# Optimization experiments

Hardware: AMD Instinct MI355X
Metric: run time of the kernel (lower is better)

## Reference

```python
import math
import jax, jax.numpy as jnp
import numpy as np

D_MODEL = 2048
NUM_EXPERTS = 64
Z_LOSS_COEF = 1e-3
AUX_LOSS_COEF = 1e-2
CAPACITY_FACTOR = 1.0
MIN_CAPACITY = 4


def setup_inputs() -> dict:
    key = jax.random.key(0)
    kx, kw = jax.random.split(key)
    x = jax.random.normal(kx, (4, 4096, D_MODEL), dtype=jnp.float32)
    W = 0.02 * jax.random.normal(kw, (NUM_EXPERTS, D_MODEL), dtype=jnp.float32)  # gate weight [E, D]
    return {"x": x, "W": W}


def reference(x, W):
    B, T, D = x.shape
    N = B * T                      # num_tokens
    E = W.shape[0]
    x_flat = x.reshape(N, D)

    logits = jnp.einsum("nd,ed->ne", x_flat, W)          # gate GEMM [N, E]
    probs = jax.nn.softmax(logits, axis=-1)

    # z-loss: mean(logsumexp(logits)^2)
    z_loss = jnp.mean(jnp.square(jax.nn.logsumexp(logits, axis=-1)))

    expert_index = jnp.argmax(logits, axis=-1)            # [N] int
    expert_prob = jnp.take_along_axis(probs, expert_index[:, None], axis=-1)[:, 0]  # [N]

    counts = jnp.bincount(expert_index, length=E)         # [E] int
    f_i = counts.astype(probs.dtype) / N                  # fraction routed per expert
    p_i = jnp.mean(probs, axis=0)                         # mean router prob per expert
    aux_loss = AUX_LOSS_COEF * E * jnp.sum(f_i * p_i) + Z_LOSS_COEF * z_loss

    capacity = max(MIN_CAPACITY, math.ceil(CAPACITY_FACTOR * N / E))  # static int
    return expert_index, expert_prob, counts, capacity, aux_loss
```

## Files before the change

### kernel.cpp

```cpp
#include <hip/hip_runtime.h>
#include <math.h>

#define D_MODEL 2048
#define NE      64
#define TB      64
#define KSEG    1024
#define KC      64
#define NCH     (KSEG / KC)
#define FB_KC   32
#define FB_NCH  (D_MODEL / FB_KC)

typedef _Float16 half8 __attribute__((ext_vector_type(8)));
typedef float    f32x4 __attribute__((ext_vector_type(4)));

#define CVT1(F, HV, LV, J) do {                                               \
    float _f = (F);                                                           \
    _Float16 _h = (_Float16)_f;                                               \
    HV[J] = _h;                                                               \
    LV[J] = (_Float16)(_f - (float)_h);                                       \
} while (0)

__global__ __launch_bounds__(256) void wcvt_kernel(
    const float* __restrict__ W, short* __restrict__ Wh, short* __restrict__ Wl)
{
    const int e = blockIdx.x, t = threadIdx.x, c = t * 8;
    const float* src = W + (size_t)e * D_MODEL + c;
    float4 v0 = *(const float4*)src;
    float4 v1 = *(const float4*)(src + 4);
    half8 hv, lv;
    CVT1(v0.x * 64.0f, hv, lv, 0); CVT1(v0.y * 64.0f, hv, lv, 1);
    CVT1(v0.z * 64.0f, hv, lv, 2); CVT1(v0.w * 64.0f, hv, lv, 3);
    CVT1(v1.x * 64.0f, hv, lv, 4); CVT1(v1.y * 64.0f, hv, lv, 5);
    CVT1(v1.z * 64.0f, hv, lv, 6); CVT1(v1.w * 64.0f, hv, lv, 7);
    *(half8*)(Wh + (size_t)e * D_MODEL + c) = hv;
    *(half8*)(Wl + (size_t)e * D_MODEL + c) = lv;
}

__global__ __launch_bounds__(512) void router_fused_db(
    const float* __restrict__ x, const short* __restrict__ Whg,
    const short* __restrict__ Wlg, float* __restrict__ out,
    float* __restrict__ ws_prob, float* __restrict__ ws_z,
    int* __restrict__ ws_cnt, int Ntok)
{
    __shared__ __align__(16) char smem[131072];

    const int t  = threadIdx.x;
    const int b  = blockIdx.x;
    const int m0 = b * TB;
    const int g  = t >> 8;
    const int tg = t & 255;
    const int l  = tg & 63;
    const int wv = tg >> 6;
    const int k0 = g * KSEG;

    char* gbase = smem + g * 65536;

    float (*sL)[NE + 1] = (float (*)[NE + 1])smem;
    float (*red8)[8]    = (float (*)[8])(smem + 16640);
    int   (*arg8)[8]    = (int (*)[8])(smem + 18688);
    float* smax         = (float*)(smem + 20736);
    float* sinv         = (float*)(smem + 20992);
    float (*spart)[NE]  = (float (*)[NE])(smem + 21248);
    int*   hist         = (int*)(smem + 23296);

    const int srow = tg >> 2;
    const int sc   = tg & 3;
    const int ssw  = srow & 7;
    const int sof0 = (srow << 6) + (((sc * 2 + 0) ^ ssw) << 3);
    const int sof1 = (srow << 6) + (((sc * 2 + 1) ^ ssw) << 3);

    float4 aA0, aA1, aA2, aA3;
    float4 aB0, aB1, aB2, aB3;
    uint4  whA0, whA1, wlA0, wlA1;
    uint4  whB0, whB1, wlB0, wlB1;

#define PRE_SET(A0, A1, A2, A3, WH0, WH1, WL0, WL1, KB) do {                  \
    const float* _ap = x + (size_t)(m0 + srow) * D_MODEL + (KB) + sc * 16;    \
    A0 = *(const float4*)_ap;       A1 = *(const float4*)(_ap + 4);           \
    A2 = *(const float4*)(_ap + 8); A3 = *(const float4*)(_ap + 12);          \
    const size_t _wr = (size_t)srow * D_MODEL + (KB) + sc * 16;               \
    WH0 = *(const uint4*)&Whg[_wr]; WH1 = *(const uint4*)&Whg[_wr + 8];       \
    WL0 = *(const uint4*)&Wlg[_wr]; WL1 = *(const uint4*)&Wlg[_wr + 8];       \
} while (0)

#define STORE_SET(A0, A1, A2, A3, WH0, WH1, WL0, WL1, BB) do {                \
    _Float16* _Ah = (_Float16*)(gbase + (BB) * 32768);                        \
    _Float16* _Al = (_Float16*)(gbase + (BB) * 32768 + 8192);                 \
    _Float16* _Wh = (_Float16*)(gbase + (BB) * 32768 + 16384);                \
    _Float16* _Wl = (_Float16*)(gbase + (BB) * 32768 + 24576);                \
    half8 _h0, _l0, _h1, _l1;                                                 \
    CVT1((A0).x * 8.0f, _h0, _l0, 0); CVT1((A0).y * 8.0f, _h0, _l0, 1);       \
    CVT1((A0).z * 8.0f, _h0, _l0, 2); CVT1((A0).w * 8.0f, _h0, _l0, 3);       \
    CVT1((A1).x * 8.0f, _h0, _l0, 4); CVT1((A1).y * 8.0f, _h0, _l0, 5);       \
    CVT1((A1).z * 8.0f, _h0, _l0, 6); CVT1((A1).w * 8.0f, _h0, _l0, 7);       \
    CVT1((A2).x * 8.0f, _h1, _l1, 0); CVT1((A2).y * 8.0f, _h1, _l1, 1);       \
    CVT1((A2).z * 8.0f, _h1, _l1, 2); CVT1((A2).w * 8.0f, _h1, _l1, 3);       \
    CVT1((A3).x * 8.0f, _h1, _l1, 4); CVT1((A3).y * 8.0f, _h1, _l1, 5);       \
    CVT1((A3).z * 8.0f, _h1, _l1, 6); CVT1((A3).w * 8.0f, _h1, _l1, 7);       \
    *(half8*)&_Ah[sof0] = _h0;  *(half8*)&_Ah[sof1] = _h1;                    \
    *(half8*)&_Al[sof0] = _l0;  *(half8*)&_Al[sof1] = _l1;                    \
    *(uint4*)&_Wh[sof0] = WH0;  *(uint4*)&_Wh[sof1] = WH1;                    \
    *(uint4*)&_Wl[sof0] = WL0;  *(uint4*)&_Wl[sof1] = WL1;                    \
} while (0)

#define MFMA_PHASE(BB) do {                                                   \
    const _Float16* _Ah = (const _Float16*)(gbase + (BB) * 32768);            \
    const _Float16* _Al = (const _Float16*)(gbase + (BB) * 32768 + 8192);     \
    const _Float16* _Wh = (const _Float16*)(gbase + (BB) * 32768 + 16384);    \
    const _Float16* _Wl = (const _Float16*)(gbase + (BB) * 32768 + 24576);    \
    const int arow = wv * 16 + (l & 15);                                      \
    const int rsw  = l & 7;                                                   \
    _Pragma("unroll")                                                         \
    for (int kq = 0; kq < 2; ++kq) {                                          \
        const int s    = kq * 4 + (l >> 4);                                   \
        const int aoff = arow * 64 + ((s ^ rsw) << 3);                        \
        half8 ah = *(const half8*)&_Ah[aoff];                                 \
        half8 al = *(const half8*)&_Al[aoff];                                 \
        _Pragma("unroll")                                                     \
        for (int n = 0; n < 4; ++n) {                                         \
            const int woff = (n * 16 + (l & 15)) * 64 + ((s ^ rsw) << 3);     \
            half8 wh = *(const half8*)&_Wh[woff];                             \
            half8 wl = *(const half8*)&_Wl[woff];                             \
            f32x4 a = (n == 0) ? acc0 : (n == 1) ? acc1 : (n == 2) ? acc2 : acc3; \
            a = __builtin_amdgcn_mfma_f32_16x16x32_f16(al, wl, a, 0, 0, 0);   \
            a = __builtin_amdgcn_mfma_f32_16x16x32_f16(al, wh, a, 0, 0, 0);   \
            a = __builtin_amdgcn_mfma_f32_16x16x32_f16(ah, wl, a, 0, 0, 0);   \
            a = __builtin_amdgcn_mfma_f32_16x16x32_f16(ah, wh, a, 0, 0, 0);   \
            if (n == 0) acc0 = a; else if (n == 1) acc1 = a;                  \
            else if (n == 2) acc2 = a; else acc3 = a;                         \
        }                                                                     \
    }                                                                         \
} while (0)

    f32x4 acc0 = {0.f,0.f,0.f,0.f}, acc1 = {0.f,0.f,0.f,0.f};
    f32x4 acc2 = {0.f,0.f,0.f,0.f}, acc3 = {0.f,0.f,0.f,0.f};

    PRE_SET(aA0, aA1, aA2, aA3, whA0, whA1, wlA0, wlA1, k0);
    PRE_SET(aB0, aB1, aB2, aB3, whB0, whB1, wlB0, wlB1, k0 + KC);
    STORE_SET(aA0, aA1, aA2, aA3, whA0, whA1, wlA0, wlA1, 0);
    asm volatile("s_waitcnt lgkmcnt(0)" ::: "memory");
    __builtin_amdgcn_s_barrier();

    for (int ch = 0; ch < NCH; ch += 2) {
        if (ch + 2 < NCH)
            PRE_SET(aA0, aA1, aA2, aA3, whA0, whA1, wlA0, wlA1, k0 + (ch + 2) * KC);
        if (ch + 1 < NCH)
            STORE_SET(aB0, aB1, aB2, aB3, whB0, whB1, wlB0, wlB1, 1);
        MFMA_PHASE(0);
        asm volatile("s_waitcnt lgkmcnt(0)" ::: "memory");
        __builtin_amdgcn_s_barrier();
        if (ch + 3 < NCH)
            PRE_SET(aB0, aB1, aB2, aB3, whB0, whB1, wlB0, wlB1, k0 + (ch + 3) * KC);
        if (ch + 2 < NCH)
            STORE_SET(aA0, aA1, aA2, aA3, whA0, whA1, wlA0, wlA1, 0);
        MFMA_PHASE(1);
        asm volatile("s_waitcnt lgkmcnt(0)" ::: "memory");
        __builtin_amdgcn_s_barrier();
    }

    __syncthreads();
    const int rbase = wv * 16 + (l >> 4) * 4;
    const int col0  = l & 15;
    if (g == 1) {
        #pragma unroll
        for (int q = 0; q < 4; ++q) {
            sL[rbase + q][ 0 + col0] = acc0[q];
            sL[rbase + q][16 + col0] = acc1[q];
            sL[rbase + q][32 + col0] = acc2[q];
            sL[rbase + q][48 + col0] = acc3[q];
        }
    }
    __syncthreads();
    if (g == 0) {
        #pragma unroll
        for (int q = 0; q < 4; ++q) {
            sL[rbase + q][ 0 + col0] = (acc0[q] + sL[rbase + q][ 0 + col0]) * (1.0f / 512.0f);
            sL[rbase + q][16 + col0] = (acc1[q] + sL[rbase + q][16 + col0]) * (1.0f / 512.0f);
            sL[rbase + q][32 + col0] = (acc2[q] + sL[rbase + q][32 + col0]) * (1.0f / 512.0f);
            sL[rbase + q][48 + col0] = (acc3[q] + sL[rbase + q][48 + col0]) * (1.0f / 512.0f);
        }
    }
    if (t < NE) hist[t] = 0;
    __syncthreads();

    {
        const int m = t >> 3, qr = t & 7;
        float mx = -3.4e38f; int ag = qr * 8;
        #pragma unroll
        for (int k = 0; k < 8; ++k) {
            const int e = qr * 8 + k;
            float v = sL[m][e];
            if (v > mx) { mx = v; ag = e; }
        }
        red8[m][qr] = mx; arg8[m][qr] = ag;
    }
    __syncthreads();
    if (t < 64) {
        const int m = t;
        float mx = red8[m][0]; int ag = arg8[m][0];
        #pragma unroll
        for (int qr = 1; qr < 8; ++qr)
            if (red8[m][qr] > mx) { mx = red8[m][qr]; ag = arg8[m][qr]; }
        smax[m] = mx;
        out[m0 + m] = (float)ag;
        atomicAdd(&hist[ag], 1);
    }
    __syncthreads();
    {
        const int m = t >> 3, qr = t & 7;
        const float mx = smax[m];
        float s = 0.f;
        #pragma unroll
        for (int k = 0; k < 8; ++k) s += expf(sL[m][qr * 8 + k] - mx);
        red8[m][qr] = s;
    }
    __syncthreads();
    if (t < 64) {
        const int m = t;
        float s = 0.f;
        #pragma unroll
        for (int qr = 0; qr < 8; ++qr) s += red8[m][qr];
        float inv = 1.f / s;
        sinv[m] = inv;
        out[Ntok + m0 + m] = inv;
        float lse = smax[m] + logf(s);
        float z = lse * lse;
        #pragma unroll
        for (int off = 32; off > 0; off >>= 1) z += __shfl_down(z, off, 64);
        if (t == 0) ws_z[b] = z;
    }
    __syncthreads();
    {
        const int e = t & 63, gw = t >> 6;
        float pa = 0.f;
        #pragma unroll
        for (int k = 0; k < 8; ++k) {
            const int m = gw * 8 + k;
            pa += expf(sL[m][e] - smax[m]) * sinv[m];
        }
        spart[gw][e] = pa;
    }
    __syncthreads();
    if (t < NE) {
        float ps = 0.f;
        #pragma unroll
        for (int gw = 0; gw < 8; ++gw) ps += spart[gw][t];
        ws_prob[b * NE + t] = ps;
        ws_cnt[b * NE + t]  = hist[t];
    }
}

__global__ __launch_bounds__(256) void router_final2(
    const float* __restrict__ ws_prob, const float* __restrict__ ws_z,
    const int* __restrict__ ws_cnt, float* __restrict__ out,
    int Ntok, int nblocks)
{
    __shared__ float sp[4][NE];
    __shared__ int   sc[4][NE];
    __shared__ float sz[4];

    const int e = threadIdx.x & 63, g = threadIdx.x >> 6;
    const int per = nblocks / 4;
    const int hi  = (g == 3) ? nblocks : (g + 1) * per;

    float ps = 0.f; int c = 0;
    for (int blk = g * per; blk < hi; ++blk) {
        ps += ws_prob[blk * NE + e];
        c  += ws_cnt[blk * NE + e];
    }
    sp[g][e] = ps; sc[g][e] = c;

    float z = 0.f;
    for (int blk = (int)threadIdx.x; blk < nblocks; blk += 256) z += ws_z[blk];
    #pragma unroll
    for (int off = 32; off > 0; off >>= 1) z += __shfl_down(z, off, 64);
    if (e == 0) sz[g] = z;
    __syncthreads();

    if (threadIdx.x < 64) {
        const int ee = threadIdx.x;
        float pst = ((sp[0][ee] + sp[1][ee]) + sp[2][ee]) + sp[3][ee];
        int   ct  = ((sc[0][ee] + sc[1][ee]) + sc[2][ee]) + sc[3][ee];
        out[2 * Ntok + ee] = (float)ct;

        float fN = (float)Ntok;
        float fp = ((float)ct / fN) * (pst / fN);
        #pragma unroll
        for (int off = 32; off > 0; off >>= 1) fp += __shfl_down(fp, off, 64);
        if (ee == 0) {
            float zt = ((sz[0] + sz[1]) + sz[2]) + sz[3];
            int cap = (Ntok + NE - 1) / NE;
            if (cap < 4) cap = 4;
            float aux = 0.01f * (float)NE * fp + 1e-3f * (zt / fN);
            out[2 * Ntok + NE]     = (float)cap;
            out[2 * Ntok + NE + 1] = aux;
        }
    }
}

__global__ __launch_bounds__(256) void router_main_fb(
    const float* __restrict__ x, const float* __restrict__ W,
    float* __restrict__ out, float* __restrict__ ws_prob,
    float* __restrict__ ws_z, int* __restrict__ ws_cnt, int Ntok)
{
    __shared__ __align__(16) float sX[FB_KC][68];
    __shared__ __align__(16) float sW[FB_KC][68];
    __shared__ float sL[64][65];
    __shared__ float smax[64], sinv[64];
    __shared__ float spart[4][NE];
    __shared__ int   hist[NE];

    const int t = threadIdx.x, b = blockIdx.x, m0 = b * 64;
    const int mq = t & 15, nq = t >> 4;
    const int r1 = t >> 3, r2 = r1 + 32, c1 = (t & 7) << 2;
    const float* xp1 = x + (size_t)(m0 + r1) * D_MODEL + c1;
    const float* xp2 = x + (size_t)(m0 + r2) * D_MODEL + c1;
    const float* wp1 = W + (size_t)r1 * D_MODEL + c1;
    const float* wp2 = W + (size_t)r2 * D_MODEL + c1;
    float4 ax1 = *(const float4*)xp1, ax2 = *(const float4*)xp2;
    float4 aw1 = *(const float4*)wp1, aw2 = *(const float4*)wp2;
    float a1[4][4] = {}, a2[4][4] = {};
    for (int ch = 0; ch < FB_NCH; ++ch) {
        __syncthreads();
        sX[c1+0][r1] = ax1.x; sX[c1+1][r1] = ax1.y; sX[c1+2][r1] = ax1.z; sX[c1+3][r1] = ax1.w;
        sX[c1+0][r2] = ax2.x; sX[c1+1][r2] = ax2.y; sX[c1+2][r2] = ax2.z; sX[c1+3][r2] = ax2.w;
        sW[c1+0][r1] = aw1.x; sW[c1+1][r1] = aw1.y; sW[c1+2][r1] = aw1.z; sW[c1+3][r1] = aw1.w;
        sW[c1+0][r2] = aw2.x; sW[c1+1][r2] = aw2.y; sW[c1+2][r2] = aw2.z; sW[c1+3][r2] = aw2.w;
        __syncthreads();
        if (ch + 1 < FB_NCH) {
            xp1 += FB_KC; xp2 += FB_KC; wp1 += FB_KC; wp2 += FB_KC;
            ax1 = *(const float4*)xp1; ax2 = *(const float4*)xp2;
            aw1 = *(const float4*)wp1; aw2 = *(const float4*)wp2;
        }
        #pragma unroll
        for (int k = 0; k < FB_KC; ++k) {
            float4 xa = *(const float4*)&sX[k][mq << 2];
            float4 wb = *(const float4*)&sW[k][nq << 2];
            float (*A)[4] = (k < FB_KC / 2) ? a1 : a2;
            A[0][0] = fmaf(xa.x, wb.x, A[0][0]); A[0][1] = fmaf(xa.x, wb.y, A[0][1]);
            A[0][2] = fmaf(xa.x, wb.z, A[0][2]); A[0][3] = fmaf(xa.x, wb.w, A[0][3]);
            A[1][0] = fmaf(xa.y, wb.x, A[1][0]); A[1][1] = fmaf(xa.y, wb.y, A[1][1]);
            A[1][2] = fmaf(xa.y, wb.z, A[1][2]); A[1][3] = fmaf(xa.y, wb.w, A[1][3]);
            A[2][0] = fmaf(xa.z, wb.x, A[2][0]); A[2][1] = fmaf(xa.z, wb.y, A[2][1]);
            A[2][2] = fmaf(xa.z, wb.z, A[2][2]); A[2][3] = fmaf(xa.z, wb.w, A[2][3]);
            A[3][0] = fmaf(xa.w, wb.x, A[3][0]); A[3][1] = fmaf(xa.w, wb.y, A[3][1]);
            A[3][2] = fmaf(xa.w, wb.z, A[3][2]); A[3][3] = fmaf(xa.w, wb.w, A[3][3]);
        }
    }
    #pragma unroll
    for (int i = 0; i < 4; ++i)
        #pragma unroll
        for (int j = 0; j < 4; ++j)
            sL[(mq << 2) + i][(nq << 2) + j] = a1[i][j] + a2[i][j];
    if (t < NE) hist[t] = 0;
    __syncthreads();
    if (t < 64) {
        const int m = t;
        float mx = sL[m][0]; int arg = 0;
        for (int e = 1; e < NE; ++e) { float v = sL[m][e]; if (v > mx) { mx = v; arg = e; } }
        float s = 0.f;
        for (int e = 0; e < NE; ++e) s += expf(sL[m][e] - mx);
        float inv = 1.f / s;
        out[m0 + m] = (float)arg; out[Ntok + m0 + m] = inv;
        smax[m] = mx; sinv[m] = inv;
        atomicAdd(&hist[arg], 1);
        float lse = mx + logf(s); float z = lse * lse;
        for (int off = 32; off > 0; off >>= 1) z += __shfl_down(z, off, 64);
        if (t == 0) ws_z[b] = z;
    }
    __syncthreads();
    {
        const int e = t & 63, mg = t >> 6;
        float pa = 0.f;
        for (int m = mg * 16; m < mg * 16 + 16; ++m) pa += expf(sL[m][e] - smax[m]) * sinv[m];
        spart[mg][e] = pa;
    }
    __syncthreads();
    if (t < NE) {
        ws_prob[b * NE + t] = spart[0][t] + spart[1][t] + spart[2][t] + spart[3][t];
        ws_cnt[b * NE + t]  = hist[t];
    }
}

extern "C" void kernel_launch(void* const* d_in, const int* in_sizes, int n_in,
                              void* d_out, int out_size, void* d_ws, size_t ws_size,
                              hipStream_t stream)
{
    const float* x = (const float*)d_in[0];
    const float* W = (const float*)d_in[1];
    float* out = (float*)d_out;

    const int Ntok = in_sizes[0] / D_MODEL;
    const int nblk = Ntok / TB;

    const size_t wh_elems = (size_t)NE * D_MODEL;
    const size_t need = wh_elems * 2 * 2
                      + ((size_t)nblk * NE + nblk) * 4
                      + (size_t)nblk * NE * 4 + 1024;

    if ((Ntok % TB) == 0 && (nblk % 4) == 0 && ws_size >= need) {
        short* wsh     = (short*)d_ws;
        short* wsl     = wsh + wh_elems;
        float* ws_prob = (float*)(wsl + wh_elems);
        float* ws_z    = ws_prob + (size_t)nblk * NE;
        int*   ws_cnt  = (int*)(ws_z + nblk);

        wcvt_kernel<<<NE, 256, 0, stream>>>(W, wsh, wsl);
        router_fused_db<<<nblk, 512, 0, stream>>>(x, wsh, wsl, out,
                                                  ws_prob, ws_z, ws_cnt, Ntok);
        router_final2<<<1, 256, 0, stream>>>(ws_prob, ws_z, ws_cnt, out, Ntok, nblk);
    } else {
        const int nb = Ntok / 64;
        float* ws_prob = (float*)d_ws;
        float* ws_z    = ws_prob + (size_t)nb * NE;
        int*   ws_cnt  = (int*)(ws_z + nb);
        router_main_fb<<<nb, 256, 0, stream>>>(x, W, out, ws_prob, ws_z, ws_cnt, Ntok);
        router_final2<<<1, 256, 0, stream>>>(ws_prob, ws_z, ws_cnt, out, Ntok, nb);
    }
}
```

Measured before the change: 59.61 us.

## Load GEMM operands directly into registers, dropping the LDS staging buffers

Removes the 128KB shared-memory double buffer and its barriers. Each lane now loads its x fragment and W hi/lo fragments straight from global memory into MFMA operand registers, with register-level double buffering across k-steps. With much smaller LDS use and launch_bounds(512,2), two blocks can reside per CU. The trade-off is that W is re-read from global or cache by every wave instead of being shared through LDS, and the global loads are less coalesced.

```diff
diff --git a/kernel.cpp b/kernel.cpp
--- a/kernel.cpp
+++ b/kernel.cpp
@@ -4,9 +4,8 @@
 #define D_MODEL 2048
 #define NE      64
 #define TB      64
-#define KSEG    1024
-#define KC      64
-#define NCH     (KSEG / KC)
+#define KHALF   1024
+#define NKS     (KHALF / 32)
 #define FB_KC   32
 #define FB_NCH  (D_MODEL / FB_KC)
 
@@ -36,13 +35,18 @@
     *(half8*)(Wl + (size_t)e * D_MODEL + c) = lv;
 }
 
-__global__ __launch_bounds__(512) void router_fused_db(
+__global__ __launch_bounds__(512, 2) void router_fused_nl(
     const float* __restrict__ x, const short* __restrict__ Whg,
     const short* __restrict__ Wlg, float* __restrict__ out,
     float* __restrict__ ws_prob, float* __restrict__ ws_z,
     int* __restrict__ ws_cnt, int Ntok)
 {
-    __shared__ __align__(16) char smem[131072];
+    __shared__ float sL[64][NE + 1];
+    __shared__ float red8[64][8];
+    __shared__ int   arg8[64][8];
+    __shared__ float smax[64], sinv[64];
+    __shared__ float spart[8][NE];
+    __shared__ int   hist[NE];
 
     const int t  = threadIdx.x;
     const int b  = blockIdx.x;
@@ -51,111 +55,66 @@
     const int tg = t & 255;
     const int l  = tg & 63;
     const int wv = tg >> 6;
-    const int k0 = g * KSEG;
-
-    char* gbase = smem + g * 65536;
-
-    float (*sL)[NE + 1] = (float (*)[NE + 1])smem;
-    float (*red8)[8]    = (float (*)[8])(smem + 16640);
-    int   (*arg8)[8]    = (int (*)[8])(smem + 18688);
-    float* smax         = (float*)(smem + 20736);
-    float* sinv         = (float*)(smem + 20992);
-    float (*spart)[NE]  = (float (*)[NE])(smem + 21248);
-    int*   hist         = (int*)(smem + 23296);
-
-    const int srow = tg >> 2;
-    const int sc   = tg & 3;
-    const int ssw  = srow & 7;
-    const int sof0 = (srow << 6) + (((sc * 2 + 0) ^ ssw) << 3);
-    const int sof1 = (srow << 6) + (((sc * 2 + 1) ^ ssw) << 3);
-
-    float4 aA0, aA1, aA2, aA3;
-    float4 aB0, aB1, aB2, aB3;
-    uint4  whA0, whA1, wlA0, wlA1;
-    uint4  whB0, whB1, wlB0, wlB1;
-
-#define PRE_SET(A0, A1, A2, A3, WH0, WH1, WL0, WL1, KB) do {                  \
-    const float* _ap = x + (size_t)(m0 + srow) * D_MODEL + (KB) + sc * 16;    \
-    A0 = *(const float4*)_ap;       A1 = *(const float4*)(_ap + 4);           \
-    A2 = *(const float4*)(_ap + 8); A3 = *(const float4*)(_ap + 12);          \
-    const size_t _wr = (size_t)srow * D_MODEL + (KB) + sc * 16;               \
-    WH0 = *(const uint4*)&Whg[_wr]; WH1 = *(const uint4*)&Whg[_wr + 8];       \
-    WL0 = *(const uint4*)&Wlg[_wr]; WL1 = *(const uint4*)&Wlg[_wr + 8];       \
-} while (0)
-
-#define STORE_SET(A0, A1, A2, A3, WH0, WH1, WL0, WL1, BB) do {                \
-    _Float16* _Ah = (_Float16*)(gbase + (BB) * 32768);                        \
-    _Float16* _Al = (_Float16*)(gbase + (BB) * 32768 + 8192);                 \
-    _Float16* _Wh = (_Float16*)(gbase + (BB) * 32768 + 16384);                \
-    _Float16* _Wl = (_Float16*)(gbase + (BB) * 32768 + 24576);                \
-    half8 _h0, _l0, _h1, _l1;                                                 \
-    CVT1((A0).x * 8.0f, _h0, _l0, 0); CVT1((A0).y * 8.0f, _h0, _l0, 1);       \
-    CVT1((A0).z * 8.0f, _h0, _l0, 2); CVT1((A0).w * 8.0f, _h0, _l0, 3);       \
-    CVT1((A1).x * 8.0f, _h0, _l0, 4); CVT1((A1).y * 8.0f, _h0, _l0, 5);       \
-    CVT1((A1).z * 8.0f, _h0, _l0, 6); CVT1((A1).w * 8.0f, _h0, _l0, 7);       \
-    CVT1((A2).x * 8.0f, _h1, _l1, 0); CVT1((A2).y * 8.0f, _h1, _l1, 1);       \
-    CVT1((A2).z * 8.0f, _h1, _l1, 2); CVT1((A2).w * 8.0f, _h1, _l1, 3);       \
-    CVT1((A3).x * 8.0f, _h1, _l1, 4); CVT1((A3).y * 8.0f, _h1, _l1, 5);       \
-    CVT1((A3).z * 8.0f, _h1, _l1, 6); CVT1((A3).w * 8.0f, _h1, _l1, 7);       \
-    *(half8*)&_Ah[sof0] = _h0;  *(half8*)&_Ah[sof1] = _h1;                    \
-    *(half8*)&_Al[sof0] = _l0;  *(half8*)&_Al[sof1] = _l1;                    \
-    *(uint4*)&_Wh[sof0] = WH0;  *(uint4*)&_Wh[sof1] = WH1;                    \
-    *(uint4*)&_Wl[sof0] = WL0;  *(uint4*)&_Wl[sof1] = WL1;                    \
-} while (0)
-
-#define MFMA_PHASE(BB) do {                                                   \
-    const _Float16* _Ah = (const _Float16*)(gbase + (BB) * 32768);            \
-    const _Float16* _Al = (const _Float16*)(gbase + (BB) * 32768 + 8192);     \
-    const _Float16* _Wh = (const _Float16*)(gbase + (BB) * 32768 + 16384);    \
-    const _Float16* _Wl = (const _Float16*)(gbase + (BB) * 32768 + 24576);    \
-    const int arow = wv * 16 + (l & 15);                                      \
-    const int rsw  = l & 7;                                                   \
-    _Pragma("unroll")                                                         \
-    for (int kq = 0; kq < 2; ++kq) {                                          \
-        const int s    = kq * 4 + (l >> 4);                                   \
-        const int aoff = arow * 64 + ((s ^ rsw) << 3);                        \
-        half8 ah = *(const half8*)&_Ah[aoff];                                 \
-        half8 al = *(const half8*)&_Al[aoff];                                 \
-        _Pragma("unroll")                                                     \
-        for (int n = 0; n < 4; ++n) {                                         \
-            const int woff = (n * 16 + (l & 15)) * 64 + ((s ^ rsw) << 3);     \
-            half8 wh = *(const half8*)&_Wh[woff];                             \
-            half8 wl = *(const half8*)&_Wl[woff];                             \
-            f32x4 a = (n == 0) ? acc0 : (n == 1) ? acc1 : (n == 2) ? acc2 : acc3; \
-            a = __builtin_amdgcn_mfma_f32_16x16x32_f16(al, wl, a, 0, 0, 0);   \
-            a = __builtin_amdgcn_mfma_f32_16x16x32_f16(al, wh, a, 0, 0, 0);   \
-            a = __builtin_amdgcn_mfma_f32_16x16x32_f16(ah, wl, a, 0, 0, 0);   \
-            a = __builtin_amdgcn_mfma_f32_16x16x32_f16(ah, wh, a, 0, 0, 0);   \
-            if (n == 0) acc0 = a; else if (n == 1) acc1 = a;                  \
-            else if (n == 2) acc2 = a; else acc3 = a;                         \
-        }                                                                     \
-    }                                                                         \
-} while (0)
+    const int k0 = g * KHALF;
+
+    const int koff = (l >> 4) * 8;
+    const float* abase = x + (size_t)(m0 + wv * 16 + (l & 15)) * D_MODEL + k0 + koff;
+    const _Float16* whb = (const _Float16*)Whg + (size_t)(l & 15) * D_MODEL + k0 + koff;
+    const _Float16* wlb = (const _Float16*)Wlg + (size_t)(l & 15) * D_MODEL + k0 + koff;
 
     f32x4 acc0 = {0.f,0.f,0.f,0.f}, acc1 = {0.f,0.f,0.f,0.f};
     f32x4 acc2 = {0.f,0.f,0.f,0.f}, acc3 = {0.f,0.f,0.f,0.f};
 
-    PRE_SET(aA0, aA1, aA2, aA3, whA0, whA1, wlA0, wlA1, k0);
-    PRE_SET(aB0, aB1, aB2, aB3, whB0, whB1, wlB0, wlB1, k0 + KC);
-    STORE_SET(aA0, aA1, aA2, aA3, whA0, whA1, wlA0, wlA1, 0);
-    asm volatile("s_waitcnt lgkmcnt(0)" ::: "memory");
-    __builtin_amdgcn_s_barrier();
-
-    for (int ch = 0; ch < NCH; ch += 2) {
-        if (ch + 2 < NCH)
-            PRE_SET(aA0, aA1, aA2, aA3, whA0, whA1, wlA0, wlA1, k0 + (ch + 2) * KC);
-        if (ch + 1 < NCH)
-            STORE_SET(aB0, aB1, aB2, aB3, whB0, whB1, wlB0, wlB1, 1);
-        MFMA_PHASE(0);
-        asm volatile("s_waitcnt lgkmcnt(0)" ::: "memory");
-        __builtin_amdgcn_s_barrier();
-        if (ch + 3 < NCH)
-            PRE_SET(aB0, aB1, aB2, aB3, whB0, whB1, wlB0, wlB1, k0 + (ch + 3) * KC);
-        if (ch + 2 < NCH)
-            STORE_SET(aA0, aA1, aA2, aA3, whA0, whA1, wlA0, wlA1, 0);
-        MFMA_PHASE(1);
-        asm volatile("s_waitcnt lgkmcnt(0)" ::: "memory");
-        __builtin_amdgcn_s_barrier();
+    float4 aA0, aA1, aB0, aB1;
+    half8  hA0, hA1, hA2, hA3, lA0, lA1, lA2, lA3;
+    half8  hB0, hB1, hB2, hB3, lB0, lB1, lB2, lB3;
+
+#define PRE(K, PA0, PA1, H0, H1, H2, H3, L0, L1, L2, L3) do {                 \
+    const float* _a = abase + (size_t)(K) * 32;                               \
+    PA0 = *(const float4*)_a; PA1 = *(const float4*)(_a + 4);                 \
+    const _Float16* _h  = whb + (size_t)(K) * 32;                             \
+    const _Float16* _lo = wlb + (size_t)(K) * 32;                             \
+    H0 = *(const half8*)(_h);                                                 \
+    H1 = *(const half8*)(_h + 16 * D_MODEL);                                  \
+    H2 = *(const half8*)(_h + 32 * D_MODEL);                                  \
+    H3 = *(const half8*)(_h + 48 * D_MODEL);                                  \
+    L0 = *(const half8*)(_lo);                                                \
+    L1 = *(const half8*)(_lo + 16 * D_MODEL);                                 \
+    L2 = *(const half8*)(_lo + 32 * D_MODEL);                                 \
+    L3 = *(const half8*)(_lo + 48 * D_MODEL);                                 \
+} while (0)
+
+#define STEP(PA0, PA1, H0, H1, H2, H3, L0, L1, L2, L3) do {                   \
+    half8 _ah, _al;                                                           \
+    CVT1((PA0).x * 8.0f, _ah, _al, 0); CVT1((PA0).y * 8.0f, _ah, _al, 1);     \
+    CVT1((PA0).z * 8.0f, _ah, _al, 2); CVT1((PA0).w * 8.0f, _ah, _al, 3);     \
+    CVT1((PA1).x * 8.0f, _ah, _al, 4); CVT1((PA1).y * 8.0f, _ah, _al, 5);     \
+    CVT1((PA1).z * 8.0f, _ah, _al, 6); CVT1((PA1).w * 8.0f, _ah, _al, 7);     \
+    acc0 = __builtin_amdgcn_mfma_f32_16x16x32_f16(_al, L0, acc0, 0, 0, 0);    \
+    acc0 = __builtin_amdgcn_mfma_f32_16x16x32_f16(_al, H0, acc0, 0, 0, 0);    \
+    acc0 = __builtin_amdgcn_mfma_f32_16x16x32_f16(_ah, L0, acc0, 0, 0, 0);    \
+    acc0 = __builtin_amdgcn_mfma_f32_16x16x32_f16(_ah, H0, acc0, 0, 0, 0);    \
+    acc1 = __builtin_amdgcn_mfma_f32_16x16x32_f16(_al, L1, acc1, 0, 0, 0);    \
+    acc1 = __builtin_amdgcn_mfma_f32_16x16x32_f16(_al, H1, acc1, 0, 0, 0);    \
+    acc1 = __builtin_amdgcn_mfma_f32_16x16x32_f16(_ah, L1, acc1, 0, 0, 0);    \
+    acc1 = __builtin_amdgcn_mfma_f32_16x16x32_f16(_ah, H1, acc1, 0, 0, 0);    \
+    acc2 = __builtin_amdgcn_mfma_f32_16x16x32_f16(_al, L2, acc2, 0, 0, 0);    \
+    acc2 = __builtin_amdgcn_mfma_f32_16x16x32_f16(_al, H2, acc2, 0, 0, 0);    \
+    acc2 = __builtin_amdgcn_mfma_f32_16x16x32_f16(_ah, L2, acc2, 0, 0, 0);    \
+    acc2 = __builtin_amdgcn_mfma_f32_16x16x32_f16(_ah, H2, acc2, 0, 0, 0);    \
+    acc3 = __builtin_amdgcn_mfma_f32_16x16x32_f16(_al, L3, acc3, 0, 0, 0);    \
+    acc3 = __builtin_amdgcn_mfma_f32_16x16x32_f16(_al, H3, acc3, 0, 0, 0);    \
+    acc3 = __builtin_amdgcn_mfma_f32_16x16x32_f16(_ah, L3, acc3, 0, 0, 0);    \
+    acc3 = __builtin_amdgcn_mfma_f32_16x16x32_f16(_ah, H3, acc3, 0, 0, 0);    \
+} while (0)
+
+    PRE(0, aA0, aA1, hA0, hA1, hA2, hA3, lA0, lA1, lA2, lA3);
+    for (int ks = 0; ks < NKS; ks += 2) {
+        PRE(ks + 1, aB0, aB1, hB0, hB1, hB2, hB3, lB0, lB1, lB2, lB3);
+        STEP(aA0, aA1, hA0, hA1, hA2, hA3, lA0, lA1, lA2, lA3);
+        if (ks + 2 < NKS)
+            PRE(ks + 2, aA0, aA1, hA0, hA1, hA2, hA3, lA0, lA1, lA2, lA3);
+        STEP(aB0, aB1, hB0, hB1, hB2, hB3, lB0, lB1, lB2, lB3);
     }
 
     __syncthreads();
@@ -406,7 +365,7 @@
         int*   ws_cnt  = (int*)(ws_z + nblk);
 
         wcvt_kernel<<<NE, 256, 0, stream>>>(W, wsh, wsl);
-        router_fused_db<<<nblk, 512, 0, stream>>>(x, wsh, wsl, out,
+        router_fused_nl<<<nblk, 512, 0, stream>>>(x, wsh, wsl, out,
                                                   ws_prob, ws_z, ws_cnt, Ntok);
         router_final2<<<1, 256, 0, stream>>>(ws_prob, ws_z, ws_cnt, out, Ntok, nblk);
     } else {
```

Result: slower. 103.6 us (+73.7%).

## Load activations straight into MFMA fragments, stage only W in LDS

Applied to the files above, without the earlier changes.

Activations are now read from global memory directly in the per-lane MFMA fragment layout and split into fp16 hi/lo in registers, so only the gate weights go through shared memory. This halves LDS use per block (128KB to 64KB) and adds a launch-bounds min-blocks hint of 2 so two blocks can be resident per CU. In exchange, the global loads of x are less coalesced (each lane reads 32-byte strips from different rows), and more registers are live at once, which could make it harder to fit two blocks.

```diff
diff --git a/kernel.cpp b/kernel.cpp
--- a/kernel.cpp
+++ b/kernel.cpp
@@ -4,9 +4,9 @@
 #define D_MODEL 2048
 #define NE      64
 #define TB      64
-#define KSEG    1024
+#define KHALF   1024
 #define KC      64
-#define NCH     (KSEG / KC)
+#define NCH     (KHALF / KC)
 #define FB_KC   32
 #define FB_NCH  (D_MODEL / FB_KC)
 
@@ -36,13 +36,13 @@
     *(half8*)(Wl + (size_t)e * D_MODEL + c) = lv;
 }
 
-__global__ __launch_bounds__(512) void router_fused_db(
+__global__ __launch_bounds__(512, 2) void router_fused_v3(
     const float* __restrict__ x, const short* __restrict__ Whg,
     const short* __restrict__ Wlg, float* __restrict__ out,
     float* __restrict__ ws_prob, float* __restrict__ ws_z,
     int* __restrict__ ws_cnt, int Ntok)
 {
-    __shared__ __align__(16) char smem[131072];
+    __shared__ __align__(16) char smem[65536];
 
     const int t  = threadIdx.x;
     const int b  = blockIdx.x;
@@ -51,9 +51,9 @@
     const int tg = t & 255;
     const int l  = tg & 63;
     const int wv = tg >> 6;
-    const int k0 = g * KSEG;
-
-    char* gbase = smem + g * 65536;
+    const int k0 = g * KHALF;
+
+    char* gbase = smem + g * 32768;
 
     float (*sL)[NE + 1] = (float (*)[NE + 1])smem;
     float (*red8)[8]    = (float (*)[8])(smem + 16640);
@@ -68,92 +68,94 @@
     const int ssw  = srow & 7;
     const int sof0 = (srow << 6) + (((sc * 2 + 0) ^ ssw) << 3);
     const int sof1 = (srow << 6) + (((sc * 2 + 1) ^ ssw) << 3);
-
+    const size_t wsrc = (size_t)srow * D_MODEL + k0 + sc * 16;
+
+    const float* abase = x + (size_t)(m0 + wv * 16 + (l & 15)) * D_MODEL
+                           + k0 + ((l >> 4) * 8);
+
+    f32x4 acc0 = {0.f,0.f,0.f,0.f}, acc1 = {0.f,0.f,0.f,0.f};
+    f32x4 acc2 = {0.f,0.f,0.f,0.f}, acc3 = {0.f,0.f,0.f,0.f};
+
+    uint4  whA0, whA1, wlA0, wlA1;
+    uint4  whB0, whB1, wlB0, wlB1;
     float4 aA0, aA1, aA2, aA3;
     float4 aB0, aB1, aB2, aB3;
-    uint4  whA0, whA1, wlA0, wlA1;
-    uint4  whB0, whB1, wlB0, wlB1;
-
-#define PRE_SET(A0, A1, A2, A3, WH0, WH1, WL0, WL1, KB) do {                  \
-    const float* _ap = x + (size_t)(m0 + srow) * D_MODEL + (KB) + sc * 16;    \
-    A0 = *(const float4*)_ap;       A1 = *(const float4*)(_ap + 4);           \
-    A2 = *(const float4*)(_ap + 8); A3 = *(const float4*)(_ap + 12);          \
-    const size_t _wr = (size_t)srow * D_MODEL + (KB) + sc * 16;               \
-    WH0 = *(const uint4*)&Whg[_wr]; WH1 = *(const uint4*)&Whg[_wr + 8];       \
-    WL0 = *(const uint4*)&Wlg[_wr]; WL1 = *(const uint4*)&Wlg[_wr + 8];       \
+
+#define PRE_W(WH0, WH1, WL0, WL1, CH) do {                                    \
+    const size_t _o = wsrc + (size_t)(CH) * KC;                               \
+    WH0 = *(const uint4*)&Whg[_o];     WH1 = *(const uint4*)&Whg[_o + 8];     \
+    WL0 = *(const uint4*)&Wlg[_o];     WL1 = *(const uint4*)&Wlg[_o + 8];     \
 } while (0)
 
-#define STORE_SET(A0, A1, A2, A3, WH0, WH1, WL0, WL1, BB) do {                \
-    _Float16* _Ah = (_Float16*)(gbase + (BB) * 32768);                        \
-    _Float16* _Al = (_Float16*)(gbase + (BB) * 32768 + 8192);                 \
-    _Float16* _Wh = (_Float16*)(gbase + (BB) * 32768 + 16384);                \
-    _Float16* _Wl = (_Float16*)(gbase + (BB) * 32768 + 24576);                \
-    half8 _h0, _l0, _h1, _l1;                                                 \
-    CVT1((A0).x * 8.0f, _h0, _l0, 0); CVT1((A0).y * 8.0f, _h0, _l0, 1);       \
-    CVT1((A0).z * 8.0f, _h0, _l0, 2); CVT1((A0).w * 8.0f, _h0, _l0, 3);       \
-    CVT1((A1).x * 8.0f, _h0, _l0, 4); CVT1((A1).y * 8.0f, _h0, _l0, 5);       \
-    CVT1((A1).z * 8.0f, _h0, _l0, 6); CVT1((A1).w * 8.0f, _h0, _l0, 7);       \
-    CVT1((A2).x * 8.0f, _h1, _l1, 0); CVT1((A2).y * 8.0f, _h1, _l1, 1);       \
-    CVT1((A2).z * 8.0f, _h1, _l1, 2); CVT1((A2).w * 8.0f, _h1, _l1, 3);       \
-    CVT1((A3).x * 8.0f, _h1, _l1, 4); CVT1((A3).y * 8.0f, _h1, _l1, 5);       \
-    CVT1((A3).z * 8.0f, _h1, _l1, 6); CVT1((A3).w * 8.0f, _h1, _l1, 7);       \
-    *(half8*)&_Ah[sof0] = _h0;  *(half8*)&_Ah[sof1] = _h1;                    \
-    *(half8*)&_Al[sof0] = _l0;  *(half8*)&_Al[sof1] = _l1;                    \
+#define STORE_W(WH0, WH1, WL0, WL1, BB) do {                                  \
+    _Float16* _Wh = (_Float16*)(gbase + (BB) * 16384);                        \
+    _Float16* _Wl = (_Float16*)(gbase + (BB) * 16384 + 8192);                 \
     *(uint4*)&_Wh[sof0] = WH0;  *(uint4*)&_Wh[sof1] = WH1;                    \
     *(uint4*)&_Wl[sof0] = WL0;  *(uint4*)&_Wl[sof1] = WL1;                    \
 } while (0)
 
-#define MFMA_PHASE(BB) do {                                                   \
-    const _Float16* _Ah = (const _Float16*)(gbase + (BB) * 32768);            \
-    const _Float16* _Al = (const _Float16*)(gbase + (BB) * 32768 + 8192);     \
-    const _Float16* _Wh = (const _Float16*)(gbase + (BB) * 32768 + 16384);    \
-    const _Float16* _Wl = (const _Float16*)(gbase + (BB) * 32768 + 24576);    \
-    const int arow = wv * 16 + (l & 15);                                      \
-    const int rsw  = l & 7;                                                   \
+#define PRE_A(PA0, PA1, PA2, PA3, CH) do {                                    \
+    const float* _a0 = abase + (size_t)(CH) * KC;                             \
+    const float* _a1 = _a0 + 32;                                              \
+    PA0 = *(const float4*)_a0; PA1 = *(const float4*)(_a0 + 4);               \
+    PA2 = *(const float4*)_a1; PA3 = *(const float4*)(_a1 + 4);               \
+} while (0)
+
+#define MFMA_PHASE(BB, PA0, PA1, PA2, PA3) do {                               \
+    const _Float16* _Wh = (const _Float16*)(gbase + (BB) * 16384);            \
+    const _Float16* _Wl = (const _Float16*)(gbase + (BB) * 16384 + 8192);     \
+    const int _rsw = l & 7;                                                   \
     _Pragma("unroll")                                                         \
     for (int kq = 0; kq < 2; ++kq) {                                          \
-        const int s    = kq * 4 + (l >> 4);                                   \
-        const int aoff = arow * 64 + ((s ^ rsw) << 3);                        \
-        half8 ah = *(const half8*)&_Ah[aoff];                                 \
-        half8 al = *(const half8*)&_Al[aoff];                                 \
+        half8 _ah, _al;                                                       \
+        if (kq == 0) {                                                        \
+            CVT1((PA0).x * 8.0f, _ah, _al, 0); CVT1((PA0).y * 8.0f, _ah, _al, 1); \
+            CVT1((PA0).z * 8.0f, _ah, _al, 2); CVT1((PA0).w * 8.0f, _ah, _al, 3); \
+            CVT1((PA1).x * 8.0f, _ah, _al, 4); CVT1((PA1).y * 8.0f, _ah, _al, 5); \
+            CVT1((PA1).z * 8.0f, _ah, _al, 6); CVT1((PA1).w * 8.0f, _ah, _al, 7); \
+        } else {                                                              \
+            CVT1((PA2).x * 8.0f, _ah, _al, 0); CVT1((PA2).y * 8.0f, _ah, _al, 1); \
+            CVT1((PA2).z * 8.0f, _ah, _al, 2); CVT1((PA2).w * 8.0f, _ah, _al, 3); \
+            CVT1((PA3).x * 8.0f, _ah, _al, 4); CVT1((PA3).y * 8.0f, _ah, _al, 5); \
+            CVT1((PA3).z * 8.0f, _ah, _al, 6); CVT1((PA3).w * 8.0f, _ah, _al, 7); \
+        }                                                                     \
+        const int _s = kq * 4 + (l >> 4);                                     \
         _Pragma("unroll")                                                     \
         for (int n = 0; n < 4; ++n) {                                         \
-            const int woff = (n * 16 + (l & 15)) * 64 + ((s ^ rsw) << 3);     \
-            half8 wh = *(const half8*)&_Wh[woff];                             \
-            half8 wl = *(const half8*)&_Wl[woff];                             \
-            f32x4 a = (n == 0) ? acc0 : (n == 1) ? acc1 : (n == 2) ? acc2 : acc3; \
-            a = __builtin_amdgcn_mfma_f32_16x16x32_f16(al, wl, a, 0, 0, 0);   \
-            a = __builtin_amdgcn_mfma_f32_16x16x32_f16(al, wh, a, 0, 0, 0);   \
-            a = __builtin_amdgcn_mfma_f32_16x16x32_f16(ah, wl, a, 0, 0, 0);   \
-            a = __builtin_amdgcn_mfma_f32_16x16x32_f16(ah, wh, a, 0, 0, 0);   \
-            if (n == 0) acc0 = a; else if (n == 1) acc1 = a;                  \
-            else if (n == 2) acc2 = a; else acc3 = a;                         \
+            const int _row  = n * 16 + (l & 15);                              \
+            const int _woff = (_row << 6) + (((_s ^ (_row & 7))) << 3);       \
+            half8 _wh = *(const half8*)&_Wh[_woff];                           \
+            half8 _wl = *(const half8*)&_Wl[_woff];                           \
+            f32x4 _a = (n == 0) ? acc0 : (n == 1) ? acc1 : (n == 2) ? acc2 : acc3; \
+            _a = __builtin_amdgcn_mfma_f32_16x16x32_f16(_al, _wl, _a, 0, 0, 0); \
+            _a = __builtin_amdgcn_mfma_f32_16x16x32_f16(_al, _wh, _a, 0, 0, 0); \
+            _a = __builtin_amdgcn_mfma_f32_16x16x32_f16(_ah, _wl, _a, 0, 0, 0); \
+            _a = __builtin_amdgcn_mfma_f32_16x16x32_f16(_ah, _wh, _a, 0, 0, 0); \
+            if (n == 0) acc0 = _a; else if (n == 1) acc1 = _a;                \
+            else if (n == 2) acc2 = _a; else acc3 = _a;                       \
         }                                                                     \
     }                                                                         \
 } while (0)
 
-    f32x4 acc0 = {0.f,0.f,0.f,0.f}, acc1 = {0.f,0.f,0.f,0.f};
-    f32x4 acc2 = {0.f,0.f,0.f,0.f}, acc3 = {0.f,0.f,0.f,0.f};
-
-    PRE_SET(aA0, aA1, aA2, aA3, whA0, whA1, wlA0, wlA1, k0);
-    PRE_SET(aB0, aB1, aB2, aB3, whB0, whB1, wlB0, wlB1, k0 + KC);
-    STORE_SET(aA0, aA1, aA2, aA3, whA0, whA1, wlA0, wlA1, 0);
+    PRE_W(whA0, whA1, wlA0, wlA1, 0);
+    STORE_W(whA0, whA1, wlA0, wlA1, 0);
+    PRE_W(whB0, whB1, wlB0, wlB1, 1);
+    PRE_A(aA0, aA1, aA2, aA3, 0);
+    PRE_A(aB0, aB1, aB2, aB3, 1);
     asm volatile("s_waitcnt lgkmcnt(0)" ::: "memory");
     __builtin_amdgcn_s_barrier();
 
     for (int ch = 0; ch < NCH; ch += 2) {
-        if (ch + 2 < NCH)
-            PRE_SET(aA0, aA1, aA2, aA3, whA0, whA1, wlA0, wlA1, k0 + (ch + 2) * KC);
-        if (ch + 1 < NCH)
-            STORE_SET(aB0, aB1, aB2, aB3, whB0, whB1, wlB0, wlB1, 1);
-        MFMA_PHASE(0);
+        if (ch + 1 < NCH) STORE_W(whB0, whB1, wlB0, wlB1, 1);
+        if (ch + 2 < NCH) PRE_W(whA0, whA1, wlA0, wlA1, ch + 2);
+        MFMA_PHASE(0, aA0, aA1, aA2, aA3);
+        if (ch + 2 < NCH) PRE_A(aA0, aA1, aA2, aA3, ch + 2);
         asm volatile("s_waitcnt lgkmcnt(0)" ::: "memory");
         __builtin_amdgcn_s_barrier();
-        if (ch + 3 < NCH)
-            PRE_SET(aB0, aB1, aB2, aB3, whB0, whB1, wlB0, wlB1, k0 + (ch + 3) * KC);
-        if (ch + 2 < NCH)
-            STORE_SET(aA0, aA1, aA2, aA3, whA0, whA1, wlA0, wlA1, 0);
-        MFMA_PHASE(1);
+        if (ch + 2 < NCH) STORE_W(whA0, whA1, wlA0, wlA1, 0);
+        if (ch + 3 < NCH) PRE_W(whB0, whB1, wlB0, wlB1, ch + 3);
+        MFMA_PHASE(1, aB0, aB1, aB2, aB3);
+        if (ch + 3 < NCH) PRE_A(aB0, aB1, aB2, aB3, ch + 3);
         asm volatile("s_waitcnt lgkmcnt(0)" ::: "memory");
         __builtin_amdgcn_s_barrier();
     }
@@ -406,7 +408,7 @@
         int*   ws_cnt  = (int*)(ws_z + nblk);
 
         wcvt_kernel<<<NE, 256, 0, stream>>>(W, wsh, wsl);
-        router_fused_db<<<nblk, 512, 0, stream>>>(x, wsh, wsl, out,
+        router_fused_v3<<<nblk, 512, 0, stream>>>(x, wsh, wsl, out,
                                                   ws_prob, ws_z, ws_cnt, Ntok);
         router_final2<<<1, 256, 0, stream>>>(ws_prob, ws_z, ws_cnt, out, Ntok, nblk);
     } else {
```

After: 58.51 us (median of 3 runs). About the same (-1.8%).
